# Kernel tuning notes

Hardware: AMD Instinct MI355X
Metric: run time of the kernel (lower is better)

Reference implementation:

```python
import jax, jax.numpy as jnp
import numpy as np

V = 50000      # tokenizer vocab size
E = 128        # embedding_dim
H = 160        # encoder_hidden_dim (bidirectional -> 2H)
D = 196        # decoder_hidden_dim
A = 224        # attention_dim
BN = 56        # bottle_neck_dim
PAD, START, END, UNK = 0, 1, 2, 3
COV_FACTOR = 0.75


def _lstm_step(x, h, c, Wi, Wh, bi, bh):
    # torch gate order: i, f, g, o
    g = x @ Wi.T + h @ Wh.T + bi + bh
    i, f, gg, o = jnp.split(g, 4, axis=-1)
    c = jax.nn.sigmoid(f) * c + jax.nn.sigmoid(i) * jnp.tanh(gg)
    h = jax.nn.sigmoid(o) * jnp.tanh(c)
    return h, c


def _run_lstm(x_tbe, Wi, Wh, bi, bh):
    B = x_tbe.shape[1]
    Hh = Wh.shape[1]
    def step(carry, xt):
        h, c = carry
        h, c = _lstm_step(xt, h, c, Wi, Wh, bi, bh)
        return (h, c), h
    init = (jnp.zeros((B, Hh), x_tbe.dtype), jnp.zeros((B, Hh), x_tbe.dtype))
    (hT, cT), hs = jax.lax.scan(step, init, x_tbe)
    return hs, hT, cT


def setup_inputs() -> dict:
    key = jax.random.key(0)
    ks = iter(jax.random.split(key, 48))
    def rn(shape, s=0.05):
        return jax.random.normal(next(ks), shape, jnp.float32) * s
    B, Tin, Ttgt = 32, 256, 100
    inp = {
        'batch_input_ids': jax.random.randint(next(ks), (B, Tin), 0, V + 50, dtype=jnp.int32),
        'batch_target_ids': jax.random.randint(next(ks), (B, Ttgt), 0, V + 50, dtype=jnp.int32),
        'max_num_oovs': 50,
        'emb': rn((V, E), 0.1),
        # bidirectional encoder LSTM
        'Wi_f': rn((4 * H, E)), 'Wh_f': rn((4 * H, H)),
        'bi_f': jnp.zeros(4 * H), 'bh_f': jnp.zeros(4 * H),
        'Wi_b': rn((4 * H, E)), 'Wh_b': rn((4 * H, H)),
        'bi_b': jnp.zeros(4 * H), 'bh_b': jnp.zeros(4 * H),
        # enc->dec bridges
        'Weh': rn((D, 2 * H)), 'beh': jnp.zeros(D),
        'Wec': rn((D, 2 * H)), 'bec': jnp.zeros(D),
        # decoder LSTMCell
        'Wi_d': rn((4 * D, E)), 'Wh_d': rn((4 * D, D)),
        'bi_d': jnp.zeros(4 * D), 'bh_d': jnp.zeros(4 * D),
        # attention
        'Wea': rn((A, 2 * H)), 'bea': jnp.zeros(A),
        'Wda': rn((A, D)),
        'Wca': rn((A, 1)),
        'v_attn': rn((1, A)),
        # vocab projection (bottleneck)
        'W1': rn((BN, D + 2 * H)), 'b1': jnp.zeros(BN),
        'W2': rn((V - END, BN)), 'b2': jnp.zeros(V - END),
        # p_gen switch
        'Wcs': rn((1, 2 * H)), 'bcs': jnp.zeros(1),
        'Wds': rn((1, D)),
        'Wes': rn((1, E)),
    }
    return inp


def reference(batch_input_ids, batch_target_ids, max_num_oovs, emb,
              Wi_f, Wh_f, bi_f, bh_f, Wi_b, Wh_b, bi_b, bh_b,
              Weh, beh, Wec, bec, Wi_d, Wh_d, bi_d, bh_d,
              Wea, bea, Wda, Wca, v_attn, W1, b1, W2, b2,
              Wcs, bcs, Wds, Wes):
    B, Tin = batch_input_ids.shape
    # map OOV input ids to <unk> for embedding lookup
    in_mapped = jnp.where(batch_input_ids >= V, UNK, batch_input_ids)
    x_tbe = emb[in_mapped].transpose(1, 0, 2)          # [Tin,B,E]
    hs_f, hTf, cTf = _run_lstm(x_tbe, Wi_f, Wh_f, bi_f, bh_f)
    hs_b, hTb, cTb = _run_lstm(x_tbe[::-1], Wi_b, Wh_b, bi_b, bh_b)
    enc = jnp.concatenate([hs_f, hs_b[::-1]], -1).transpose(1, 0, 2)  # [B,Tin,2H]
    h = jnp.concatenate([hTf, hTb], -1) @ Weh.T + beh   # [B,D]
    c = jnp.concatenate([cTf, cTb], -1) @ Wec.T + bec   # [B,D]
    enc_attn = enc @ Wea.T + bea                        # [B,Tin,A] (loop-invariant)
    pad_mask = batch_input_ids == PAD
    wca = Wca[:, 0]                                     # [A]
    cov0 = jnp.zeros((B, Tin))
    cur0 = jnp.full((B,), START, jnp.int32)

    def step(carry, nt):
        h, c, cov, cur, nll, cl = carry
        e = emb[cur]                                     # [B,E]
        h, c = _lstm_step(e, h, c, Wi_d, Wh_d, bi_d, bh_d)
        s = jnp.tanh(enc_attn + (h @ Wda.T)[:, None, :] + cov[:, :, None] * wca)
        s = s @ v_attn[0]                                # [B,Tin]
        s = jnp.where(pad_mask, -jnp.inf, s)
        attn = jax.nn.softmax(s, axis=1)                 # [B,Tin]
        ctx = jnp.einsum('bt,bth->bh', attn, enc)        # [B,2H]
        hc = jnp.concatenate([h, ctx], -1)
        vocab = jax.nn.softmax(jnp.tanh(hc @ W1.T + b1) @ W2.T + b2, axis=1)  # [B,V-END]
        p_gen = jax.nn.sigmoid(ctx @ Wcs[0] + bcs[0] + h @ Wds[0] + e @ Wes[0])  # [B]
        # F.pad(vocab, (END, max_num_oovs)).gather(1, nt): left-pad END zeros,
        # right-pad OOV zeros -> gen prob is vocab[nt-END] if END<=nt<V else 0
        idx = jnp.clip(nt - END, 0, vocab.shape[1] - 1)
        gen_p = jnp.take_along_axis(vocab, idx[:, None], axis=1)[:, 0]
        gen_p = jnp.where((nt >= END) & (nt < V), gen_p, 0.0)
        copy_p = jnp.sum(attn * (batch_input_ids == nt[:, None]), axis=1)
        p = p_gen * gen_p + (1.0 - p_gen) * copy_p
        nll = nll - jnp.log(p + 1e-9)
        cl = cl + jnp.minimum(attn, cov).sum(axis=1)
        cov = cov + attn
        cur = jnp.where(nt >= V, UNK, nt)
        return (h, c, cov, cur, nll, cl), None

    (h, c, cov, cur, nll, cl), _ = jax.lax.scan(
        step, (h, c, cov0, cur0, jnp.zeros(B), jnp.zeros(B)), batch_target_ids.T)
    nll_loss = nll.sum()
    cov_loss = cl.sum()
    return nll_loss, cov_loss, nll_loss + COV_FACTOR * cov_loss
```

## Files before the change

kernel.cpp:

```cpp
#include <hip/hip_runtime.h>

#define MSCOPE __HIP_MEMORY_SCOPE_AGENT


constexpr size_t oXf   = 0;
constexpr size_t oXb   = oXf   + (size_t)8192*640;
constexpr size_t oXd   = oXb   + (size_t)8192*640;
constexpr size_t oHencB= oXd   + (size_t)3200*784;
constexpr size_t oEncA = oHencB+ (size_t)64*256*160;
constexpr size_t oEs   = oEncA + (size_t)8192*224;
constexpr size_t oCT   = oEs   + 3200;
constexpr size_t oH0   = oCT   + 10240;
constexpr size_t oC0   = oH0   + 6272;
constexpr size_t oHWdsAll = oC0 + 6272;
constexpr size_t oCtxWAll = oHWdsAll + 3200;
constexpr size_t oCopyAll = oCtxWAll + 3200;
constexpr size_t oZidxAll = oCopyAll + 3200;
constexpr size_t oClAll   = oZidxAll + 3200;
constexpr size_t oNllWg   = oClAll + 32;
constexpr size_t oW1cT    = oNllWg + 224;
constexpr size_t oFEnd    = oW1cT + 17920;
constexpr size_t oHdAll   = 0;
constexpr size_t oUAll    = oHdAll + (size_t)100*6272;
constexpr size_t oUPreAll = oUAll  + (size_t)100*1792;
constexpr size_t oHwdaAll = oUPreAll + (size_t)100*1792;
constexpr size_t oPartAll = oHwdaAll + (size_t)100*7168;
#define ENCW(d,t)  (((d)*256 + (t))*16)
#define FLSTM(s)   (8192 + (s)*16)
#define FAUX(s)    (9792 + (s)*16)
#define FP2W(s,m)  (11392 + (s)*64 + (m)*16)
#define CP3        17792
#define CFIN       17793
constexpr int fEnd = 17800;
constexpr unsigned ENC_FULL  = 0xFFFFFu;
constexpr unsigned LSTM_FULL = 0x1FFFFFFu;
constexpr unsigned P2_FULL   = 0xFFFFFFFFu;

__device__ __forceinline__ float fast_tanh(float x){
  float e = __expf(-2.f*fabsf(x));
  float r = (1.f - e) * __builtin_amdgcn_rcpf(1.f + e);
  return copysignf(r, x);
}
__device__ __forceinline__ float sigm(float x){
  return __builtin_amdgcn_rcpf(1.f + __expf(-x));
}
__device__ __forceinline__ float aload(const float* p){
  return __hip_atomic_load(const_cast<float*>(p), __ATOMIC_RELAXED, MSCOPE);
}
__device__ __forceinline__ float2 aload2(const float* p){
  unsigned long long u = __hip_atomic_load(
      reinterpret_cast<unsigned long long*>(const_cast<float*>(p)),
      __ATOMIC_RELAXED, MSCOPE);
  float2 r; __builtin_memcpy(&r, &u, 8); return r;
}
__device__ __forceinline__ void astore(float* p, float v){
  __hip_atomic_store(p, v, __ATOMIC_RELAXED, MSCOPE);
}
template<int SLP>
__device__ __forceinline__ void wait_mask(unsigned* word, unsigned target, int tid){
  if (tid == 0){
    while (__hip_atomic_load(word, __ATOMIC_RELAXED, MSCOPE) != target)
      __builtin_amdgcn_s_sleep(SLP);
  }
  __syncthreads();
}
__device__ __forceinline__ void or_bit(unsigned* word, unsigned bit){
  (void)__hip_atomic_fetch_or(word, bit, __ATOMIC_RELAXED, MSCOPE);
}
__device__ __forceinline__ void add1(unsigned* word){
  (void)__hip_atomic_fetch_add(word, 1u, __ATOMIC_RELAXED, MSCOPE);
}
__device__ __forceinline__ float block_sum(float v, float* red){
  #pragma unroll
  for (int o=32;o;o>>=1) v += __shfl_down(v,o);
  if ((threadIdx.x&63)==0) red[threadIdx.x>>6] = v;
  __syncthreads();
  v = red[0]+red[1]+red[2]+red[3];
  __syncthreads();
  return v;
}

__global__ void prep_kernel(const int* __restrict__ in_ids, const int* __restrict__ tgt,
                            int* __restrict__ in_mapped, int* __restrict__ cur_ids,
                            unsigned* __restrict__ flags){
  int i = blockIdx.x*256 + threadIdx.x;
  if (i < 8192){
    int t = i >> 5, b = i & 31;
    int id = in_ids[b*256 + t];
    in_mapped[i] = (id >= 50000) ? 3 : id;
  }
  if (i < 3200){
    int k = i >> 5, b = i & 31;
    int id = (k == 0) ? 1 : tgt[b*100 + (k-1)];
    cur_ids[i] = (id >= 50000) ? 3 : id;
  }
  if (i < fEnd) flags[i] = 0u;
}

__global__ void w1c_transpose(const float* __restrict__ W1, float* __restrict__ W1cT){
  int i = blockIdx.x*256 + threadIdx.x;
  if (i < 17920){ int q = i / 56, g = i - q*56; W1cT[q*56+g] = W1[(size_t)g*516 + 196 + q]; }
}

struct RGArgs{ const int* gid; const float* emb; const float* W;
               const float* bias1; const float* bias2; float* out; int N; };
__global__ void __launch_bounds__(256) rowgemm(RGArgs a){
  __shared__ float rl[8*128];
  const int tid = threadIdx.x;
  const int N = a.N;
  const size_t r0 = (size_t)blockIdx.x*8;
  for (int i = tid; i < 8*128; i += 256){
    int r = i >> 7, k = i & 127;
    rl[i] = a.emb[(size_t)a.gid[r0+r]*128 + k];
  }
  __syncthreads();
  for (int g = tid; g < N; g += 256){
    const float* wr = a.W + (size_t)g*128;
    float acc[8];
    #pragma unroll
    for (int r=0;r<8;r++) acc[r]=0.f;
    for (int k=0;k<128;k+=4){
      float4 wv = *(const float4*)(wr+k);
      #pragma unroll
      for (int r=0;r<8;r++){
        float4 xv = *(const float4*)(rl + r*128 + k);
        acc[r] += wv.x*xv.x + wv.y*xv.y + wv.z*xv.z + wv.w*xv.w;
      }
    }
    float bias = a.bias1[g] + a.bias2[g];
    #pragma unroll
    for (int r=0;r<8;r++) a.out[(r0+r)*(size_t)N + g] = acc[r] + bias;
  }
}

__global__ void es_kernel(const int* __restrict__ gid, const float* __restrict__ emb,
                          const float* __restrict__ Wes, float* __restrict__ es){
  int r = blockIdx.x, l = threadIdx.x;
  const float* e = emb + (size_t)gid[r]*128;
  float acc = e[l]*Wes[l] + e[l+64]*Wes[l+64];
  #pragma unroll
  for (int o=32;o;o>>=1) acc += __shfl_down(acc,o);
  if (l==0) es[r] = acc;
}

struct EncArgs{ const float* Xf; const float* Xb; const float* Whf; const float* Whb;
                float* hencB; float* cT; unsigned* flg; };
__global__ void __launch_bounds__(256) enc_scan(EncArgs a){
  extern __shared__ float sm[];
  float* Wl = sm;
  float* hl = sm + 5120;
  const int wg = blockIdx.x;
  const int dir = wg/20, jwg = wg%20;
  const int tid = threadIdx.x;
  const int b = tid & 31, jl = tid >> 5;
  const int j = jwg*8 + jl;
  const float* Wh = dir ? a.Whb : a.Whf;
  const float* X  = dir ? a.Xb  : a.Xf;
  float* HB = a.hencB + (size_t)dir*32*256*160;
  for (int i = tid; i < 32*160; i += 256){
    int row = i/160, k = i - row*160;
    int gate = row >> 3, jj = row & 7;
    Wl[i] = Wh[((size_t)(gate*160 + jwg*8 + jj))*160 + k];
  }
  for (int i = tid; i < 32*164; i += 256) hl[i] = 0.f;
  float c = 0.f;
  const float4* w0 = (const float4*)(Wl + (0*8+jl)*160);
  const float4* w1 = (const float4*)(Wl + (1*8+jl)*160);
  const float4* w2 = (const float4*)(Wl + (2*8+jl)*160);
  const float4* w3 = (const float4*)(Wl + (3*8+jl)*160);
  __syncthreads();
  for (int t = 0; t < 256; ++t){
    const int trow = dir ? 255 - t : t;
    const float* xr = X + ((size_t)trow*32 + b)*640 + j;
    float g0 = xr[0], g1 = xr[160], g2 = xr[320], g3 = xr[480];
    if (t > 0){
      wait_mask<2>(a.flg + ENCW(dir, t-1), ENC_FULL, tid);
      const int tprev = dir ? (256 - t) : (t-1);
      for (int i2 = tid; i2 < 2560; i2 += 256){
        int bb = i2/80, kk = (i2 - bb*80)*2;
        float2 v = aload2(HB + ((size_t)bb*256 + tprev)*160 + kk);
        *(float2*)(hl + bb*164 + kk) = v;
      }
    }
    __syncthreads();
    const float4* hr = (const float4*)(hl + b*164);
    #pragma unroll 4
    for (int q = 0; q < 40; ++q){
      float4 hv = hr[q];
      float4 a0 = w0[q], a1 = w1[q], a2 = w2[q], a3 = w3[q];
      g0 += hv.x*a0.x + hv.y*a0.y + hv.z*a0.z + hv.w*a0.w;
      g1 += hv.x*a1.x + hv.y*a1.y + hv.z*a1.z + hv.w*a1.w;
      g2 += hv.x*a2.x + hv.y*a2.y + hv.z*a2.z + hv.w*a2.w;
      g3 += hv.x*a3.x + hv.y*a3.y + hv.z*a3.z + hv.w*a3.w;
    }
    float ig = sigm(g0), fg = sigm(g1), gc = fast_tanh(g2), og = sigm(g3);
    c = fg*c + ig*gc;
    float h = og * fast_tanh(c);
    astore(&HB[((size_t)b*256 + trow)*160 + j], h);
    __syncthreads();
    if (tid == 0) or_bit(a.flg + ENCW(dir, t), 1u << jwg);
  }
  a.cT[dir*5120 + b*160 + j] = c;
}

__global__ void mid_kernel(const float* __restrict__ hencB, const float* __restrict__ cT,
                           const float* __restrict__ Weh, const float* __restrict__ beh,
                           const float* __restrict__ Wec, const float* __restrict__ bec,
                           float* __restrict__ h0, float* __restrict__ c0){
  __shared__ float hc[320], cc[320];
  int b = blockIdx.x, tid = threadIdx.x;
  if (tid < 160){
    hc[tid]     = hencB[((size_t)b*256 + 255)*160 + tid];
    hc[160+tid] = hencB[((size_t)(32+b)*256 + 0)*160 + tid];
    cc[tid]     = cT[b*160 + tid];
    cc[160+tid] = cT[5120 + b*160 + tid];
  }
  __syncthreads();
  for (int g = tid; g < 196; g += 256){
    const float* w1 = Weh + (size_t)g*320;
    const float* w2 = Wec + (size_t)g*320;
    float a1 = beh[g], a2 = bec[g];
    for (int k = 0; k < 320; ++k){ a1 += hc[k]*w1[k]; a2 += cc[k]*w2[k]; }
    h0[b*196 + g] = a1;
    c0[b*196 + g] = a2;
  }
}

__global__ void __launch_bounds__(256) encA_gemm(const float* __restrict__ hencB,
                 const float* __restrict__ Wea, const float* __restrict__ bea,
                 float* __restrict__ encA){
  __shared__ float rl[8*320];
  const int tid = threadIdx.x;
  const size_t r0 = (size_t)blockIdx.x*8;
  for (int i = tid; i < 8*320; i += 256){
    int r = i/320, k = i - r*320;
    size_t row = r0 + r; int b = (int)(row >> 8), t = (int)(row & 255);
    rl[i] = (k < 160) ? hencB[((size_t)b*256 + t)*160 + k]
                      : hencB[((size_t)(32+b)*256 + t)*160 + (k-160)];
  }
  __syncthreads();
  for (int g = tid; g < 224; g += 256){
    const float* wr = Wea + (size_t)g*320;
    float acc[8];
    #pragma unroll
    for (int r=0;r<8;r++) acc[r]=0.f;
    for (int k=0;k<320;k+=4){
      float4 wv = *(const float4*)(wr+k);
      #pragma unroll
      for (int r=0;r<8;r++){
        float4 xv = *(const float4*)(rl + r*320 + k);
        acc[r] += wv.x*xv.x + wv.y*xv.y + wv.z*xv.z + wv.w*xv.w;
      }
    }
    float bias = bea[g];
    #pragma unroll
    for (int r=0;r<8;r++) encA[(r0+r)*224 + g] = acc[r] + bias;
  }
}

struct DecArgs{
  const float* Xd; const float* hencB; const float* encA;
  const float* h0; const float* c0;
  const float* Whd; const float* Wda; const float* Wca; const float* vat;
  const float* W1; const float* b1; const float* W1cT; const float* W2; const float* b2;
  const float* Wcs; const float* bcs; const float* Wds; const float* es;
  const int* in_ids; const int* tgt;
  float* hdAll; float* uAll; float* uPreAll; float* hwdaAll;
  float* hWdsAll; float* ctxWAll; float* copyAll;
  float* zidxAll; float* partAll; float* clAll; float* nllWg; float* out;
  unsigned* flg;
};

__global__ void __launch_bounds__(256) dec_scan(DecArgs A){
  extern __shared__ float sm[];
  const int wg = blockIdx.x, tid = threadIdx.x;
  const int bp = tid & 31, jl = tid >> 5;

  if (wg >= 256){
    const int wl = wg - 256;
    const int j = wl*8 + jl;
    float* Wl   = sm;
    float* scr  = sm + 6272;
    float* wdaL = sm + 12800;
    float* w1hL = sm + 14564;
    const int na = (wl == 24) ? 8 : 9;
    const int ng = (wl < 6) ? 3 : 2;
    for (int i = tid; i < 32*196; i += 256){
      int row = i/196, k = i - row*196;
      int gate = row >> 3, jj = row & 7;
      int jg = wl*8 + jj;
      Wl[i] = (jg < 196) ? A.Whd[((size_t)(gate*196 + jg))*196 + k] : 0.f;
    }
    for (int i = tid; i < na*196; i += 256){
      int al = i/196, k = i - al*196;
      wdaL[i] = A.Wda[(size_t)(wl*9 + al)*196 + k];
    }
    for (int i = tid; i < ng*196; i += 256){
      int gl = i/196, k = i - gl*196;
      w1hL[i] = A.W1[(size_t)(wl + 25*gl)*516 + k];
    }
    float c = (j < 196) ? A.c0[bp*196 + j] : 0.f;
    for (int i = tid; i < 6272; i += 256){
      int bb = i/196, k = i - bb*196;
      scr[bb*204 + k] = A.h0[i];
    }
    const float4* w0 = (const float4*)(Wl + (0*8+jl)*196);
    const float4* w1 = (const float4*)(Wl + (1*8+jl)*196);
    const float4* w2 = (const float4*)(Wl + (2*8+jl)*196);
    const float4* w3 = (const float4*)(Wl + (3*8+jl)*196);
    __syncthreads();
    for (int s = 0; s < 100; ++s){
      if (j < 196){
        const float* xr = A.Xd + ((size_t)s*32 + bp)*784 + j;
        float g0 = xr[0], g1 = xr[196], g2 = xr[392], g3 = xr[588];
        const float4* hr = (const float4*)(scr + bp*204);
        #pragma unroll 7
        for (int q = 0; q < 49; ++q){
          float4 hv = hr[q];
          float4 a0 = w0[q], a1 = w1[q], a2 = w2[q], a3 = w3[q];
          g0 += hv.x*a0.x + hv.y*a0.y + hv.z*a0.z + hv.w*a0.w;
          g1 += hv.x*a1.x + hv.y*a1.y + hv.z*a1.z + hv.w*a1.w;
          g2 += hv.x*a2.x + hv.y*a2.y + hv.z*a2.z + hv.w*a2.w;
          g3 += hv.x*a3.x + hv.y*a3.y + hv.z*a3.z + hv.w*a3.w;
        }
        float ig = sigm(g0), fg = sigm(g1), gc = fast_tanh(g2), og = sigm(g3);
        c = fg*c + ig*gc;
        float h = og * fast_tanh(c);
        astore(&A.hdAll[(size_t)s*6272 + bp*196 + j], h);
      }
      __syncthreads();
      if (tid == 0) or_bit(A.flg + FLSTM(s), 1u << wl);
      wait_mask<2>(A.flg + FLSTM(s), LSTM_FULL, tid);
      {
        const float* hp = A.hdAll + (size_t)s*6272;
        for (int i2 = tid; i2 < 3136; i2 += 256){
          float2 hv2 = aload2(hp + i2*2);
          int bb = i2/98, kk = (i2 - bb*98)*2;
          *(float2*)(scr + bb*204 + kk) = hv2;
        }
      }
      __syncthreads();
      for (int i = tid; i < na*32; i += 256){
        int al = i >> 5, bb = i & 31;
        const float4* h4 = (const float4*)(scr + bb*204);
        const float4* w4 = (const float4*)(wdaL + al*196);
        float acc = 0.f;
        #pragma unroll 7
        for (int q = 0; q < 49; ++q){
          float4 a4 = h4[q], b4 = w4[q];
          acc += a4.x*b4.x + a4.y*b4.y + a4.z*b4.z + a4.w*b4.w;
        }
        astore(&A.hwdaAll[(size_t)s*7168 + bb*224 + wl*9 + al], acc);
      }
      for (int i = tid; i < ng*32; i += 256){
        int gl = i >> 5, bb = i & 31;
        int g = wl + 25*gl;
        const float4* h4 = (const float4*)(scr + bb*204);
        const float4* w4 = (const float4*)(w1hL + gl*196);
        float acc = A.b1[g];
        #pragma unroll 7
        for (int q = 0; q < 49; ++q){
          float4 a4 = h4[q], b4 = w4[q];
          acc += a4.x*b4.x + a4.y*b4.y + a4.z*b4.z + a4.w*b4.w;
        }
        astore(&A.uPreAll[(size_t)s*1792 + bb*56 + g], acc);
      }
      if (wl == 24 && tid < 32){
        const float* hb = scr + tid*204;
        float acc = 0.f;
        #pragma unroll 4
        for (int q = 0; q < 196; ++q) acc += hb[q]*A.Wds[q];
        astore(&A.hWdsAll[s*32 + tid], acc);
      }
      __syncthreads();
      if (tid == 0) or_bit(A.flg + FAUX(s), 1u << wl);
    }
    return;
  }

  if (wg < 32){
    const int b = wg;
    float* hwdaL = sm;
    float* attnL = sm + 224;
    float* pctx  = sm + 480;
    float* ctxL  = sm + 1440;
    float* red   = sm + 1760;
    float* pu    = sm + 1764;
    float* wcaL  = sm + 1988;
    float* vL    = sm + 2212;
    float* WcsL  = sm + 2436;
    if (tid < 224){ wcaL[tid] = A.Wca[tid]; vL[tid] = A.vat[tid]; }
    for (int i = tid; i < 320; i += 256) WcsL[i] = A.Wcs[i];
    const int inid = A.in_ids[b*256 + tid];
    const float4* erow = (const float4*)(A.encA + (size_t)(b*256 + tid)*224);
    float cov = 0.f, clr = 0.f;
    __syncthreads();
    for (int s = 0; s < 100; ++s){
      wait_mask<2>(A.flg + FAUX(s), LSTM_FULL, tid);
      if (tid < 224) hwdaL[tid] = aload(&A.hwdaAll[(size_t)s*7168 + b*224 + tid]);
      __syncthreads();
      float exv = 0.f;
      if (inid != 0){
        float acc = 0.f;
        #pragma unroll 8
        for (int q = 0; q < 56; ++q){
          float4 ev = erow[q]; int a0 = 4*q;
          acc += fast_tanh(ev.x + hwdaL[a0]   + cov*wcaL[a0]  )*vL[a0];
          acc += fast_tanh(ev.y + hwdaL[a0+1] + cov*wcaL[a0+1])*vL[a0+1];
          acc += fast_tanh(ev.z + hwdaL[a0+2] + cov*wcaL[a0+2])*vL[a0+2];
          acc += fast_tanh(ev.w + hwdaL[a0+3] + cov*wcaL[a0+3])*vL[a0+3];
        }
        exv = __expf(acc);
      }
      float S = block_sum(exv, red);
      float attn = exv * __builtin_amdgcn_rcpf(S);
      attnL[tid] = attn;
      const int ntb = A.tgt[b*100 + s];
      float cpS = block_sum((inid == ntb) ? attn : 0.f, red);
      float mnS = block_sum(fminf(attn, cov), red);
      if (tid == 0){
        astore(&A.copyAll[s*32 + b], cpS);
        clr += mnS;
        if (s == 99) astore(&A.clAll[b], clr);
      }
      cov += attn;
      if (tid < 240){
        int seg = tid/80, h4i = tid - seg*80;
        int t0 = seg*86, t1 = (t0+86 < 256) ? t0+86 : 256;
        const float* base = (h4i < 40)
          ? (A.hencB + ((size_t)b*256)*160 + (size_t)h4i*4)
          : (A.hencB + ((size_t)(32+b)*256)*160 + (size_t)(h4i-40)*4);
        float4 accv = {0.f,0.f,0.f,0.f};
        #pragma unroll 4
        for (int t2 = t0; t2 < t1; ++t2){
          float av = attnL[t2];
          float4 ev = *(const float4*)(base + (size_t)t2*160);
          accv.x += av*ev.x; accv.y += av*ev.y; accv.z += av*ev.z; accv.w += av*ev.w;
        }
        *(float4*)(pctx + (seg*80+h4i)*4) = accv;
      }
      __syncthreads();
      if (tid < 80){
        float4 p0 = *(float4*)(pctx + tid*4);
        float4 p1 = *(float4*)(pctx + (80+tid)*4);
        float4 p2v = *(float4*)(pctx + (160+tid)*4);
        float4 cvv;
        cvv.x = p0.x+p1.x+p2v.x; cvv.y = p0.y+p1.y+p2v.y;
        cvv.z = p0.z+p1.z+p2v.z; cvv.w = p0.w+p1.w+p2v.w;
        *(float4*)(ctxL + tid*4) = cvv;
      }
      __syncthreads();
      if (tid < 224){
        int g = tid % 56, seg = tid / 56;
        float acc = 0.f;
        const float* wp = A.W1cT + (size_t)seg*80*56 + g;
        #pragma unroll 4
        for (int q = 0; q < 80; ++q) acc += ctxL[seg*80 + q] * wp[q*56];
        pu[seg*56 + g] = acc;
      } else {
        int l = tid - 224; float acc = 0.f;
        for (int q = l; q < 320; q += 32) acc += ctxL[q]*WcsL[q];
        #pragma unroll
        for (int o=16;o;o>>=1) acc += __shfl_down(acc,o,32);
        if (l==0) astore(&A.ctxWAll[s*32 + b], acc);
      }
      __syncthreads();
      if (tid < 56){
        float upre = aload(&A.uPreAll[(size_t)s*1792 + b*56 + tid]);
        float uu = fast_tanh(upre + pu[tid] + pu[56+tid] + pu[112+tid] + pu[168+tid]);
        astore(&A.uAll[(size_t)s*1792 + b*56 + tid], uu);
      }
      __syncthreads();
      if (tid == 0){
        or_bit(A.flg + FP2W(s,0), 1u << b);
        or_bit(A.flg + FP2W(s,1), 1u << b);
        or_bit(A.flg + FP2W(s,2), 1u << b);
        or_bit(A.flg + FP2W(s,3), 1u << b);
      }
    }
    return;
  }

  {
    const int wgv = wg - 32;
    const int vs = (wgv*49998)/224, ve = ((wgv+1)*49998)/224;
    const int v = vs + tid;
    const bool valid = v < ve;
    const int vc = valid ? v : 0;
    float4 w2r[14];
    {
      const float4* wr = (const float4*)(A.W2 + (size_t)vc*56);
      #pragma unroll
      for (int q=0;q<14;++q) w2r[q] = wr[q];
    }
    const float b2v = A.b2[vc];
    float* ulL  = sm;
    float* redW = sm + 1792;
    int*   idxL = (int*)(sm + 1920);
    float* red  = sm + 1952;
    const int lane = tid & 63, wv2 = tid >> 6;
    for (int s = 0; s < 100; ++s){
      int nt3 = (tid < 32) ? A.tgt[tid*100 + s] : 0;
      wait_mask<8>(A.flg + FP2W(s, wgv & 3), P2_FULL, tid);
      for (int i2 = tid; i2 < 896; i2 += 256){
        float2 u2 = aload2(&A.uAll[(size_t)s*1792 + i2*2]);
        *(float2*)(ulL + i2*2) = u2;
      }
      if (tid < 32){
        int ix = nt3 - 2; ix = ix<0?0:(ix>49997?49997:ix);
        idxL[tid] = ix;
      }
      __syncthreads();
      #pragma unroll 4
      for (int bb=0; bb<32; ++bb){
        const float4* uv = (const float4*)(ulL + bb*56);
        float z = b2v;
        #pragma unroll
        for (int q=0;q<14;++q){
          float4 u4 = uv[q];
          z += w2r[q].x*u4.x + w2r[q].y*u4.y + w2r[q].z*u4.z + w2r[q].w*u4.w;
        }
        if (valid && v == idxL[bb]) astore(&A.zidxAll[s*32+bb], z);
        float sv2 = valid ? __expf(z) : 0.f;
        #pragma unroll
        for (int o=32;o;o>>=1) sv2 += __shfl_down(sv2,o);
        if (lane == 0) redW[wv2*32+bb] = sv2;
      }
      __syncthreads();
      if (tid < 32){
        float tot = redW[tid]+redW[32+tid]+redW[64+tid]+redW[96+tid];
        astore(&A.partAll[(size_t)(s*32+tid)*224 + wgv], tot);
      }
      __syncthreads();
    }
    __syncthreads();
    if (tid == 0) add1(A.flg + CP3);
    if (tid == 0){
      while (__hip_atomic_load(A.flg + CP3, __ATOMIC_RELAXED, MSCOPE) != 224u)
        __builtin_amdgcn_s_sleep(32);
    }
    __syncthreads();
    float nll1 = 0.f;
    for (int p = wgv; p < 3200; p += 224){
      float pv = (tid < 224) ? aload(&A.partAll[(size_t)p*224 + tid]) : 0.f;
      float se = block_sum(pv, red);
      if (tid == 0){
        int s = p >> 5, b = p & 31;
        int nt2 = A.tgt[b*100 + s];
        float xg = aload(&A.ctxWAll[p]) + A.bcs[0] + aload(&A.hWdsAll[p]) + A.es[p];
        float pg = 1.f/(1.f + __expf(-xg));
        float genp = (nt2 >= 2 && nt2 < 50000) ? (__expf(aload(&A.zidxAll[p])) / se) : 0.f;
        float pr = pg*genp + (1.f-pg)*aload(&A.copyAll[p]);
        nll1 += -logf(pr + 1e-9f);
      }
    }
    if (tid == 0) astore(&A.nllWg[wgv], nll1);
    __syncthreads();
    if (tid == 0) add1(A.flg + CFIN);
    if (wg == 32){
      if (tid == 0){
        while (__hip_atomic_load(A.flg + CFIN, __ATOMIC_RELAXED, MSCOPE) != 224u)
          __builtin_amdgcn_s_sleep(32);
      }
      __syncthreads();
      float nv = (tid < 224) ? aload(&A.nllWg[tid]) : 0.f;
      float nll = block_sum(nv, red);
      float cv = (tid < 32) ? aload(&A.clAll[tid]) : 0.f;
      float cl = block_sum(cv, red);
      if (tid == 0){ A.out[0]=nll; A.out[1]=cl; A.out[2]=nll + 0.75f*cl; }
    }
  }
}

extern "C" void kernel_launch(void* const* d_in, const int* in_sizes, int n_in,
                              void* d_out, int out_size, void* d_ws, size_t ws_size,
                              hipStream_t stream){
  const int*   in_ids = (const int*)  d_in[0];
  const int*   tgt    = (const int*)  d_in[1];
  const float* emb    = (const float*)d_in[3];
  const float* Wi_f   = (const float*)d_in[4];
  const float* Wh_f   = (const float*)d_in[5];
  const float* bi_f   = (const float*)d_in[6];
  const float* bh_f   = (const float*)d_in[7];
  const float* Wi_b   = (const float*)d_in[8];
  const float* Wh_b   = (const float*)d_in[9];
  const float* bi_b   = (const float*)d_in[10];
  const float* bh_b   = (const float*)d_in[11];
  const float* Weh    = (const float*)d_in[12];
  const float* beh    = (const float*)d_in[13];
  const float* Wec    = (const float*)d_in[14];
  const float* bec    = (const float*)d_in[15];
  const float* Wi_d   = (const float*)d_in[16];
  const float* Wh_d   = (const float*)d_in[17];
  const float* bi_d   = (const float*)d_in[18];
  const float* bh_d   = (const float*)d_in[19];
  const float* Wea    = (const float*)d_in[20];
  const float* bea    = (const float*)d_in[21];
  const float* Wda    = (const float*)d_in[22];
  const float* Wca    = (const float*)d_in[23];
  const float* vat    = (const float*)d_in[24];
  const float* W1     = (const float*)d_in[25];
  const float* b1     = (const float*)d_in[26];
  const float* W2     = (const float*)d_in[27];
  const float* b2     = (const float*)d_in[28];
  const float* Wcs    = (const float*)d_in[29];
  const float* bcs    = (const float*)d_in[30];
  const float* Wds    = (const float*)d_in[31];
  const float* Wes    = (const float*)d_in[32];

  float* ws = (float*)d_ws;
  int* iBase = (int*)(ws + oFEnd);
  int* in_mapped = iBase;
  int* cur_ids   = iBase + 8192;
  unsigned* flags = (unsigned*)(iBase + 11392);

  prep_kernel<<<128, 256, 0, stream>>>(in_ids, tgt, in_mapped, cur_ids, flags);
  w1c_transpose<<<70, 256, 0, stream>>>(W1, ws + oW1cT);

  { RGArgs a{in_mapped, emb, Wi_f, bi_f, bh_f, ws + oXf, 640};
    rowgemm<<<1024, 256, 0, stream>>>(a); }
  { RGArgs a{in_mapped, emb, Wi_b, bi_b, bh_b, ws + oXb, 640};
    rowgemm<<<1024, 256, 0, stream>>>(a); }
  { RGArgs a{cur_ids, emb, Wi_d, bi_d, bh_d, ws + oXd, 784};
    rowgemm<<<400, 256, 0, stream>>>(a); }

  es_kernel<<<3200, 64, 0, stream>>>(cur_ids, emb, Wes, ws + oEs);

  { EncArgs ea{ws + oXf, ws + oXb, Wh_f, Wh_b, ws + oHencB, ws + oCT,
               flags};
    void* ka[] = {&ea};
    hipLaunchCooperativeKernel((void*)enc_scan, dim3(40), dim3(256), ka,
                               (unsigned)((5120 + 32*164)*4), stream); }

  mid_kernel<<<32, 256, 0, stream>>>(ws + oHencB, ws + oCT, Weh, beh, Wec, bec,
                                     ws + oH0, ws + oC0);

  encA_gemm<<<1024, 256, 0, stream>>>(ws + oHencB, Wea, bea, ws + oEncA);

  { DecArgs da{ws + oXd, ws + oHencB, ws + oEncA,
               ws + oH0, ws + oC0,
               Wh_d, Wda, Wca, vat,
               W1, b1, ws + oW1cT, W2, b2, Wcs, bcs, Wds, ws + oEs,
               in_ids, tgt,
               ws + oHdAll, ws + oUAll, ws + oUPreAll, ws + oHwdaAll,
               ws + oHWdsAll, ws + oCtxWAll, ws + oCopyAll,
               ws + oZidxAll, ws + oPartAll, ws + oClAll, ws + oNllWg, (float*)d_out,
               flags};
    void* ka[] = {&da};
    hipLaunchCooperativeKernel((void*)dec_scan, dim3(281), dim3(256), ka,
                               (unsigned)(15152*4), stream); }
}
```

Before: 5.057 ms.

## Split decoder LSTM and attention-aux into separate workgroups; transpose gate-input layout

The decoder's LSTM workgroups no longer compute the attention projection, bottleneck pre-activation and p_gen term after each step. Those move to 8 dedicated aux workgroups that consume each step's hidden state in parallel, so the serial LSTM recurrence only does its own matvec and can start the next step sooner. The precomputed gate-input tensors are also laid out batch-innermost, which makes rowgemm stores float4-wide and encoder/decoder loads contiguous across lanes. In exchange the launch uses more workgroups, the aux stage sits on the critical path through its own flag wait, and the hidden-state transpose in load_scr does scattered LDS writes.

After: 4.651 ms. 1.09x faster.

```diff
diff --git a/kernel.cpp b/kernel.cpp
--- a/kernel.cpp
+++ b/kernel.cpp
@@ -34,6 +34,7 @@
 constexpr int fEnd = 17800;
 constexpr unsigned ENC_FULL  = 0xFFFFFu;
 constexpr unsigned LSTM_FULL = 0x1FFFFFFu;
+constexpr unsigned AUX_FULL  = 0xFFu;
 constexpr unsigned P2_FULL   = 0xFFFFFFFFu;
 
 __device__ __forceinline__ float fast_tanh(float x){
@@ -109,6 +110,7 @@
   const int tid = threadIdx.x;
   const int N = a.N;
   const size_t r0 = (size_t)blockIdx.x*8;
+  const size_t t = r0 >> 5; const int b0 = (int)(r0 & 31);
   for (int i = tid; i < 8*128; i += 256){
     int r = i >> 7, k = i & 127;
     rl[i] = a.emb[(size_t)a.gid[r0+r]*128 + k];
@@ -128,8 +130,9 @@
       }
     }
     float bias = a.bias1[g] + a.bias2[g];
-    #pragma unroll
-    for (int r=0;r<8;r++) a.out[(r0+r)*(size_t)N + g] = acc[r] + bias;
+    float* op = a.out + ((size_t)t*N + g)*32 + b0;
+    *(float4*)(op)   = make_float4(acc[0]+bias,acc[1]+bias,acc[2]+bias,acc[3]+bias);
+    *(float4*)(op+4) = make_float4(acc[4]+bias,acc[5]+bias,acc[6]+bias,acc[7]+bias);
   }
 }
 
@@ -157,6 +160,7 @@
   const float* Wh = dir ? a.Whb : a.Whf;
   const float* X  = dir ? a.Xb  : a.Xf;
   float* HB = a.hencB + (size_t)dir*32*256*160;
+  unsigned* flg = a.flg;
   for (int i = tid; i < 32*160; i += 256){
     int row = i/160, k = i - row*160;
     int gate = row >> 3, jj = row & 7;
@@ -171,10 +175,10 @@
   __syncthreads();
   for (int t = 0; t < 256; ++t){
     const int trow = dir ? 255 - t : t;
-    const float* xr = X + ((size_t)trow*32 + b)*640 + j;
-    float g0 = xr[0], g1 = xr[160], g2 = xr[320], g3 = xr[480];
+    const float* xr = X + ((size_t)trow*640 + j)*32 + b;
+    float g0 = xr[0], g1 = xr[5120], g2 = xr[10240], g3 = xr[15360];
     if (t > 0){
-      wait_mask<2>(a.flg + ENCW(dir, t-1), ENC_FULL, tid);
+      wait_mask<2>(flg + ENCW(dir, t-1), ENC_FULL, tid);
       const int tprev = dir ? (256 - t) : (t-1);
       for (int i2 = tid; i2 < 2560; i2 += 256){
         int bb = i2/80, kk = (i2 - bb*80)*2;
@@ -198,7 +202,7 @@
     float h = og * fast_tanh(c);
     astore(&HB[((size_t)b*256 + trow)*160 + j], h);
     __syncthreads();
-    if (tid == 0) or_bit(a.flg + ENCW(dir, t), 1u << jwg);
+    if (tid == 0) or_bit(flg + ENCW(dir, t), 1u << jwg);
   }
   a.cT[dir*5120 + b*160 + j] = c;
 }
@@ -271,34 +275,32 @@
   unsigned* flg;
 };
 
+__device__ __forceinline__ void load_scr(const float* hp, float* scr, int tid){
+  for (int i2 = tid; i2 < 3136; i2 += 256){
+    float2 hv = aload2(hp + i2*2);
+    int e = i2*2; int b2 = e & 31; int j2 = e >> 5;
+    scr[b2*204 + j2]     = hv.x;
+    scr[(b2+1)*204 + j2] = hv.y;
+  }
+}
+
 __global__ void __launch_bounds__(256) dec_scan(DecArgs A){
   extern __shared__ float sm[];
   const int wg = blockIdx.x, tid = threadIdx.x;
   const int bp = tid & 31, jl = tid >> 5;
-
-  if (wg >= 256){
-    const int wl = wg - 256;
+  unsigned* flg = A.flg;
+
+  if (wg < 25){
+    const int wl = wg;
     const int j = wl*8 + jl;
-    float* Wl   = sm;
-    float* scr  = sm + 6272;
-    float* wdaL = sm + 12800;
-    float* w1hL = sm + 14564;
-    const int na = (wl == 24) ? 8 : 9;
-    const int ng = (wl < 6) ? 3 : 2;
+    float* Wl  = sm;
+    float* scr = sm + 6272;
     for (int i = tid; i < 32*196; i += 256){
       int row = i/196, k = i - row*196;
       int gate = row >> 3, jj = row & 7;
       int jg = wl*8 + jj;
       Wl[i] = (jg < 196) ? A.Whd[((size_t)(gate*196 + jg))*196 + k] : 0.f;
     }
-    for (int i = tid; i < na*196; i += 256){
-      int al = i/196, k = i - al*196;
-      wdaL[i] = A.Wda[(size_t)(wl*9 + al)*196 + k];
-    }
-    for (int i = tid; i < ng*196; i += 256){
-      int gl = i/196, k = i - gl*196;
-      w1hL[i] = A.W1[(size_t)(wl + 25*gl)*516 + k];
-    }
     float c = (j < 196) ? A.c0[bp*196 + j] : 0.f;
     for (int i = tid; i < 6272; i += 256){
       int bb = i/196, k = i - bb*196;
@@ -310,9 +312,18 @@
     const float4* w3 = (const float4*)(Wl + (3*8+jl)*196);
     __syncthreads();
     for (int s = 0; s < 100; ++s){
+      float x0=0.f,x1=0.f,x2=0.f,x3=0.f;
       if (j < 196){
-        const float* xr = A.Xd + ((size_t)s*32 + bp)*784 + j;
-        float g0 = xr[0], g1 = xr[196], g2 = xr[392], g3 = xr[588];
+        const float* xr = A.Xd + ((size_t)s*784 + j)*32 + bp;
+        x0 = xr[0]; x1 = xr[6272]; x2 = xr[12544]; x3 = xr[18816];
+      }
+      if (s > 0){
+        wait_mask<2>(flg + FLSTM(s-1), LSTM_FULL, tid);
+        load_scr(A.hdAll + (size_t)(s-1)*6272, scr, tid);
+      }
+      __syncthreads();
+      if (j < 196){
+        float g0=x0,g1=x1,g2=x2,g3=x3;
         const float4* hr = (const float4*)(scr + bp*204);
         #pragma unroll 7
         for (int q = 0; q < 49; ++q){
@@ -326,23 +337,37 @@
         float ig = sigm(g0), fg = sigm(g1), gc = fast_tanh(g2), og = sigm(g3);
         c = fg*c + ig*gc;
         float h = og * fast_tanh(c);
-        astore(&A.hdAll[(size_t)s*6272 + bp*196 + j], h);
-      }
-      __syncthreads();
-      if (tid == 0) or_bit(A.flg + FLSTM(s), 1u << wl);
-      wait_mask<2>(A.flg + FLSTM(s), LSTM_FULL, tid);
-      {
-        const float* hp = A.hdAll + (size_t)s*6272;
-        for (int i2 = tid; i2 < 3136; i2 += 256){
-          float2 hv2 = aload2(hp + i2*2);
-          int bb = i2/98, kk = (i2 - bb*98)*2;
-          *(float2*)(scr + bb*204 + kk) = hv2;
-        }
-      }
-      __syncthreads();
-      for (int i = tid; i < na*32; i += 256){
-        int al = i >> 5, bb = i & 31;
-        const float4* h4 = (const float4*)(scr + bb*204);
+        astore(&A.hdAll[(size_t)s*6272 + j*32 + bp], h);
+      }
+      __syncthreads();
+      if (tid == 0) or_bit(flg + FLSTM(s), 1u << wl);
+    }
+    return;
+  }
+
+  if (wg < 33){
+    const int a_ = wg - 25;
+    float* wdaL = sm;
+    float* w1hL = sm + 5488;
+    float* WdsL = sm + 6860;
+    float* scr  = sm + 7056;
+    for (int i = tid; i < 28*196; i += 256){
+      int al = i/196, k = i - al*196;
+      wdaL[i] = A.Wda[(size_t)(a_*28 + al)*196 + k];
+    }
+    for (int i = tid; i < 7*196; i += 256){
+      int gl = i/196, k = i - gl*196;
+      w1hL[i] = A.W1[(size_t)(a_*7 + gl)*516 + k];
+    }
+    if (a_ == 7) for (int i = tid; i < 196; i += 256) WdsL[i] = A.Wds[i];
+    __syncthreads();
+    for (int s = 0; s < 100; ++s){
+      wait_mask<2>(flg + FLSTM(s), LSTM_FULL, tid);
+      load_scr(A.hdAll + (size_t)s*6272, scr, tid);
+      __syncthreads();
+      for (int i = tid; i < 896; i += 256){
+        int b2 = i & 31, al = i >> 5;
+        const float4* h4 = (const float4*)(scr + b2*204);
         const float4* w4 = (const float4*)(wdaL + al*196);
         float acc = 0.f;
         #pragma unroll 7
@@ -350,12 +375,12 @@
           float4 a4 = h4[q], b4 = w4[q];
           acc += a4.x*b4.x + a4.y*b4.y + a4.z*b4.z + a4.w*b4.w;
         }
-        astore(&A.hwdaAll[(size_t)s*7168 + bb*224 + wl*9 + al], acc);
-      }
-      for (int i = tid; i < ng*32; i += 256){
-        int gl = i >> 5, bb = i & 31;
-        int g = wl + 25*gl;
-        const float4* h4 = (const float4*)(scr + bb*204);
+        astore(&A.hwdaAll[(size_t)s*7168 + b2*224 + a_*28 + al], acc);
+      }
+      if (tid < 224){
+        int b2 = tid & 31, gl = tid >> 5;
+        int g = a_*7 + gl;
+        const float4* h4 = (const float4*)(scr + b2*204);
         const float4* w4 = (const float4*)(w1hL + gl*196);
         float acc = A.b1[g];
         #pragma unroll 7
@@ -363,23 +388,23 @@
           float4 a4 = h4[q], b4 = w4[q];
           acc += a4.x*b4.x + a4.y*b4.y + a4.z*b4.z + a4.w*b4.w;
         }
-        astore(&A.uPreAll[(size_t)s*1792 + bb*56 + g], acc);
-      }
-      if (wl == 24 && tid < 32){
+        astore(&A.uPreAll[(size_t)s*1792 + b2*56 + g], acc);
+      }
+      if (a_ == 7 && tid < 32){
         const float* hb = scr + tid*204;
         float acc = 0.f;
         #pragma unroll 4
-        for (int q = 0; q < 196; ++q) acc += hb[q]*A.Wds[q];
+        for (int q = 0; q < 196; ++q) acc += hb[q]*WdsL[q];
         astore(&A.hWdsAll[s*32 + tid], acc);
       }
       __syncthreads();
-      if (tid == 0) or_bit(A.flg + FAUX(s), 1u << wl);
+      if (tid == 0) or_bit(flg + FAUX(s), 1u << a_);
     }
     return;
   }
 
-  if (wg < 32){
-    const int b = wg;
+  if (wg < 65){
+    const int b = wg - 33;
     float* hwdaL = sm;
     float* attnL = sm + 224;
     float* pctx  = sm + 480;
@@ -396,7 +421,7 @@
     float cov = 0.f, clr = 0.f;
     __syncthreads();
     for (int s = 0; s < 100; ++s){
-      wait_mask<2>(A.flg + FAUX(s), LSTM_FULL, tid);
+      wait_mask<2>(flg + FAUX(s), AUX_FULL, tid);
       if (tid < 224) hwdaL[tid] = aload(&A.hwdaAll[(size_t)s*7168 + b*224 + tid]);
       __syncthreads();
       float exv = 0.f;
@@ -472,17 +497,17 @@
       }
       __syncthreads();
       if (tid == 0){
-        or_bit(A.flg + FP2W(s,0), 1u << b);
-        or_bit(A.flg + FP2W(s,1), 1u << b);
-        or_bit(A.flg + FP2W(s,2), 1u << b);
-        or_bit(A.flg + FP2W(s,3), 1u << b);
+        or_bit(flg + FP2W(s,0), 1u << b);
+        or_bit(flg + FP2W(s,1), 1u << b);
+        or_bit(flg + FP2W(s,2), 1u << b);
+        or_bit(flg + FP2W(s,3), 1u << b);
       }
     }
     return;
   }
 
   {
-    const int wgv = wg - 32;
+    const int wgv = wg - 65;
     const int vs = (wgv*49998)/224, ve = ((wgv+1)*49998)/224;
     const int v = vs + tid;
     const bool valid = v < ve;
@@ -501,7 +526,7 @@
     const int lane = tid & 63, wv2 = tid >> 6;
     for (int s = 0; s < 100; ++s){
       int nt3 = (tid < 32) ? A.tgt[tid*100 + s] : 0;
-      wait_mask<8>(A.flg + FP2W(s, wgv & 3), P2_FULL, tid);
+      wait_mask<8>(flg + FP2W(s, wgv & 3), P2_FULL, tid);
       for (int i2 = tid; i2 < 896; i2 += 256){
         float2 u2 = aload2(&A.uAll[(size_t)s*1792 + i2*2]);
         *(float2*)(ulL + i2*2) = u2;
@@ -534,9 +559,9 @@
       __syncthreads();
     }
     __syncthreads();
-    if (tid == 0) add1(A.flg + CP3);
+    if (tid == 0) add1(flg + CP3);
     if (tid == 0){
-      while (__hip_atomic_load(A.flg + CP3, __ATOMIC_RELAXED, MSCOPE) != 224u)
+      while (__hip_atomic_load(flg + CP3, __ATOMIC_RELAXED, MSCOPE) != 224u)
         __builtin_amdgcn_s_sleep(32);
     }
     __syncthreads();
@@ -556,10 +581,10 @@
     }
     if (tid == 0) astore(&A.nllWg[wgv], nll1);
     __syncthreads();
-    if (tid == 0) add1(A.flg + CFIN);
-    if (wg == 32){
+    if (tid == 0) add1(flg + CFIN);
+    if (wg == 65){
       if (tid == 0){
-        while (__hip_atomic_load(A.flg + CFIN, __ATOMIC_RELAXED, MSCOPE) != 224u)
+        while (__hip_atomic_load(flg + CFIN, __ATOMIC_RELAXED, MSCOPE) != 224u)
           __builtin_amdgcn_s_sleep(32);
       }
       __syncthreads();
@@ -626,8 +651,7 @@
 
   es_kernel<<<3200, 64, 0, stream>>>(cur_ids, emb, Wes, ws + oEs);
 
-  { EncArgs ea{ws + oXf, ws + oXb, Wh_f, Wh_b, ws + oHencB, ws + oCT,
-               flags};
+  { EncArgs ea{ws + oXf, ws + oXb, Wh_f, Wh_b, ws + oHencB, ws + oCT, flags};
     void* ka[] = {&ea};
     hipLaunchCooperativeKernel((void*)enc_scan, dim3(40), dim3(256), ka,
                                (unsigned)((5120 + 32*164)*4), stream); }
@@ -647,6 +671,6 @@
                ws + oZidxAll, ws + oPartAll, ws + oClAll, ws + oNllWg, (float*)d_out,
                flags};
     void* ka[] = {&da};
-    hipLaunchCooperativeKernel((void*)dec_scan, dim3(281), dim3(256), ka,
-                               (unsigned)(15152*4), stream); }
-}
+    hipLaunchCooperativeKernel((void*)dec_scan, dim3(289), dim3(256), ka,
+                               (unsigned)(13584*4), stream); }
+}
```
